# Kernel optimization log

Measured on AMD Instinct MI355X. Metric: run time of the kernel, lower is better.

Reference implementation:

```python
import jax, jax.numpy as jnp
import numpy as np

B, L, IN_DIM, D_MODEL, N_LAYERS = 4, 1024, 64, 512, 3
D_INNER, STATE, DT_RANK, K = 1024, 16, 32, 4  # expand=2, dt_rank=d_model//16, conv kernel 4


def setup_inputs() -> dict:
    key = jax.random.key(0)
    ks = jax.random.split(key, 8)
    s = 0.02
    def rn(k, shp):
        return jax.random.normal(k, shp, jnp.float32) * s
    inp = {"x": jax.random.normal(ks[0], (B, L, IN_DIM), jnp.float32)}
    inp["input_w"] = rn(ks[1], (D_MODEL, IN_DIM)); inp["input_b"] = jnp.zeros((D_MODEL,), jnp.float32)
    inp["in_proj_w"] = rn(ks[2], (N_LAYERS, 2 * D_INNER, D_MODEL)); inp["in_proj_b"] = jnp.zeros((N_LAYERS, 2 * D_INNER), jnp.float32)
    inp["conv_w"] = rn(ks[3], (N_LAYERS, D_INNER, 1, K)); inp["conv_b"] = jnp.zeros((N_LAYERS, D_INNER), jnp.float32)
    inp["x_proj_w"] = rn(ks[4], (N_LAYERS, DT_RANK + 2 * STATE, D_INNER))
    inp["dt_proj_w"] = rn(ks[5], (N_LAYERS, D_INNER, DT_RANK)); inp["dt_proj_b"] = jnp.full((N_LAYERS, D_INNER), -4.0, jnp.float32)
    inp["A_log"] = jnp.tile(jnp.log(jnp.arange(1, STATE + 1, dtype=jnp.float32))[None, None, :], (N_LAYERS, D_INNER, 1))
    inp["D"] = jnp.ones((N_LAYERS, D_INNER), jnp.float32)
    inp["out_proj_w"] = rn(ks[6], (N_LAYERS, D_MODEL, D_INNER)); inp["out_proj_b"] = jnp.zeros((N_LAYERS, D_MODEL), jnp.float32)
    inp["ln_w"] = jnp.ones((N_LAYERS, D_MODEL), jnp.float32); inp["ln_b"] = jnp.zeros((N_LAYERS, D_MODEL), jnp.float32)
    return inp


def _layernorm(x, w, b):
    mu = jnp.mean(x, -1, keepdims=True)
    v = jnp.var(x, -1, keepdims=True)
    return (x - mu) * jax.lax.rsqrt(v + 1e-5) * w + b


def _mamba(u, iw, ib, cw, cb, xw, dw, db, A_log, Dp, ow, ob):
    # u: [B, L, d_model]
    xz = u @ iw.T + ib                          # [B, L, 2*d_inner]
    xp, z = jnp.split(xz, 2, axis=-1)
    # causal depthwise conv over time
    xc = jax.lax.conv_general_dilated(xp.transpose(0, 2, 1), cw, (1,), [(K - 1, 0)],
                                      feature_group_count=D_INNER,
                                      dimension_numbers=("NCH", "OIH", "NCH")) + cb[None, :, None]
    xc = jax.nn.silu(xc).transpose(0, 2, 1)     # [B, L, d_inner]
    proj = xc @ xw.T                            # [B, L, dt_rank + 2*N]
    dtl = proj[..., :DT_RANK]
    Bm = proj[..., DT_RANK:DT_RANK + STATE]
    Cm = proj[..., DT_RANK + STATE:]
    dt = jax.nn.softplus(dtl @ dw.T + db)       # [B, L, d_inner]
    A = -jnp.exp(A_log)                         # [d_inner, N]

    def step(h, t):
        dt_t, B_t, C_t, x_t = t                 # [B,d], [B,N], [B,N], [B,d]
        h = h * jnp.exp(dt_t[..., None] * A) + (dt_t * x_t)[..., None] * B_t[:, None, :]
        return h, jnp.einsum("bdn,bn->bd", h, C_t)

    h0 = jnp.zeros((u.shape[0], D_INNER, STATE), u.dtype)
    _, ys = jax.lax.scan(step, h0, (dt.transpose(1, 0, 2), Bm.transpose(1, 0, 2),
                                    Cm.transpose(1, 0, 2), xc.transpose(1, 0, 2)))
    y = ys.transpose(1, 0, 2) + xc * Dp
    y = y * jax.nn.silu(z)
    return y @ ow.T + ob


def reference(x, input_w, input_b, in_proj_w, in_proj_b, conv_w, conv_b, x_proj_w,
              dt_proj_w, dt_proj_b, A_log, D, out_proj_w, out_proj_b, ln_w, ln_b):
    h = x @ input_w.T + input_b                 # [B, L, d_model]
    for i in range(N_LAYERS):
        res = h
        h = _mamba(h, in_proj_w[i], in_proj_b[i], conv_w[i], conv_b[i], x_proj_w[i],
                   dt_proj_w[i], dt_proj_b[i], A_log[i], D[i], out_proj_w[i], out_proj_b[i])
        h = _layernorm(h + res, ln_w[i], ln_b[i])
    return h[:, -1, :]
```

## Files before the change

### kernel.cpp

```cpp
#include <hip/hip_runtime.h>
#include <hip/hip_bf16.h>
#include <cstddef>
#include <cstdint>

#define NB 4
#define NL 1024
#define IN_DIM 64
#define D_MODEL 512
#define N_LAYERS 3
#define D_INNER 1024
#define NSTATE 16
#define DT_RANK 32
#define KCONV 4
#define NROWS (NB * NL)
#define CHUNK 16
#define NCHUNK (NL / CHUNK)
#define LOG2E 1.4426950408889634f

typedef __attribute__((ext_vector_type(8))) short short8;
typedef __attribute__((ext_vector_type(4))) float f32x4;
typedef __attribute__((ext_vector_type(4))) unsigned short us4;
typedef unsigned short ushort_t;

__device__ __forceinline__ ushort_t f2b1(float x) {
  uint32_t u = __builtin_bit_cast(uint32_t, x);
  u += 0x7fffu + ((u >> 16) & 1u);
  return (ushort_t)(u >> 16);
}
__device__ __forceinline__ float b2f(ushort_t u) {
  return __builtin_bit_cast(float, (uint32_t)u << 16);
}

__device__ __forceinline__ void gload_lds16(const ushort_t* src, short* dst) {
  __builtin_amdgcn_global_load_lds(
      (const __attribute__((address_space(1))) uint32_t*)src,
      (__attribute__((address_space(3))) uint32_t*)dst, 16, 0, 0);
}

#define E0 (NROWS * IN_DIM)
#define E1 (D_MODEL * IN_DIM)
#define E2 (N_LAYERS * 2 * D_INNER * D_MODEL)
#define E3 (N_LAYERS * 64 * D_INNER)
#define E4 (N_LAYERS * D_INNER * DT_RANK)
#define E5 (N_LAYERS * D_MODEL * D_INNER)
#define ETOT (E0 + E1 + E2 + E3 + E4 + E5)

__global__ __launch_bounds__(256) void cvt_all(
    const float* __restrict__ x, const float* __restrict__ inw,
    const float* __restrict__ ipw, const float* __restrict__ xpw,
    const float* __restrict__ dpw, const float* __restrict__ opw,
    ushort_t* __restrict__ xb, ushort_t* __restrict__ inwb,
    ushort_t* __restrict__ iwb, ushort_t* __restrict__ xwb,
    ushort_t* __restrict__ dwb, ushort_t* __restrict__ owb)
{
  int i = (blockIdx.x * 256 + threadIdx.x) * 4;
  if (i >= ETOT) return;
  const float* src; ushort_t* dst; int off;
  if      (i < E0)                  { src = x;   dst = xb;   off = i; }
  else if (i < E0+E1)               { src = inw; dst = inwb; off = i - E0; }
  else if (i < E0+E1+E2)            { src = ipw; dst = iwb;  off = i - (E0+E1); }
  else if (i < E0+E1+E2+E3)         { src = xpw; dst = xwb;  off = i - (E0+E1+E2); }
  else if (i < E0+E1+E2+E3+E4)      { src = dpw; dst = dwb;  off = i - (E0+E1+E2+E3); }
  else                              { src = opw; dst = owb;  off = i - (E0+E1+E2+E3+E4); }
  const float4 v = *(const float4*)(src + off);
  us4 o;
  o.x = f2b1(v.x); o.y = f2b1(v.y); o.z = f2b1(v.z); o.w = f2b1(v.w);
  *(us4*)(dst + off) = o;
}

template<int BM, int BN, int MF, int NF, int ACT, bool WF32, bool WB16>
__global__ __launch_bounds__(256) void gemm_mfma(
    const ushort_t* __restrict__ A, int lda,
    const ushort_t* __restrict__ W,
    const float* __restrict__ bias,
    float* __restrict__ Cf, ushort_t* __restrict__ Cb,
    int M, int N, int K)
{
  constexpr int CA = BM / 64;
  constexpr int CB = BN / 64;
  __shared__ __align__(16) short sa[BM * 32];
  __shared__ __align__(16) short sb[BN * 32];

  const int tid = threadIdx.x;
  const int l = tid & 63;
  const int wid = tid >> 6;
  const int wrow = (wid >> 1) * (BM / 2);
  const int wcol = (wid & 1) * (BN / 2);
  const int m0 = blockIdx.y * BM;
  const int n0 = blockIdx.x * BN;

  const int srow = l >> 2;
  const int scol = (l & 3) * 8;

  f32x4 acc[MF][NF] = {};

  for (int k0 = 0; k0 < K; k0 += 32) {
#pragma unroll
    for (int c = 0; c < CA; ++c) {
      short* dst = sa + (c * 4 + wid) * 512;
      const ushort_t* src =
          A + (size_t)(m0 + (c * 4 + wid) * 16 + srow) * lda + k0 + scol;
      gload_lds16(src, dst);
    }
#pragma unroll
    for (int c = 0; c < CB; ++c) {
      short* dst = sb + (c * 4 + wid) * 512;
      const ushort_t* src =
          W + (size_t)(n0 + (c * 4 + wid) * 16 + srow) * K + k0 + scol;
      gload_lds16(src, dst);
    }
    __syncthreads();

    short8 af[MF], bfr[NF];
#pragma unroll
    for (int mi = 0; mi < MF; ++mi)
      af[mi] = *(const short8*)(sa + (wrow + mi * 16 + (l & 15)) * 32 + (l >> 4) * 8);
#pragma unroll
    for (int nj = 0; nj < NF; ++nj)
      bfr[nj] = *(const short8*)(sb + (wcol + nj * 16 + (l & 15)) * 32 + (l >> 4) * 8);
#pragma unroll
    for (int mi = 0; mi < MF; ++mi)
#pragma unroll
      for (int nj = 0; nj < NF; ++nj)
        acc[mi][nj] = __builtin_amdgcn_mfma_f32_16x16x32_bf16(
            af[mi], bfr[nj], acc[mi][nj], 0, 0, 0);
    __syncthreads();
  }

#pragma unroll
  for (int nj = 0; nj < NF; ++nj) {
    const int col = n0 + wcol + nj * 16 + (l & 15);
    const float bv = bias ? bias[col] : 0.f;
#pragma unroll
    for (int mi = 0; mi < MF; ++mi) {
#pragma unroll
      for (int q = 0; q < 4; ++q) {
        const int row = m0 + wrow + mi * 16 + (l >> 4) * 4 + q;
        float v = acc[mi][nj][q] + bv;
        if (ACT == 1) v = (v > 20.f) ? v : log1pf(__expf(v));
        if (WF32) Cf[(size_t)row * N + col] = v;
        if (WB16) Cb[(size_t)row * N + col] = f2b1(v);
      }
    }
  }
}

__global__ __launch_bounds__(256) void conv_silu(
    const ushort_t* __restrict__ xzb,
    const float* __restrict__ cw,
    const float* __restrict__ cb,
    ushort_t* __restrict__ xcb)
{
  const int idx = blockIdx.x * 256 + threadIdx.x;
  const int d4 = (idx & (D_INNER / 4 - 1)) * 4;
  const int bt = idx >> 8;
  const int t = bt & (NL - 1);
  const int b = bt >> 10;

  float acc4[4];
  {
    const float4 cbv = *(const float4*)(cb + d4);
    acc4[0] = cbv.x; acc4[1] = cbv.y; acc4[2] = cbv.z; acc4[3] = cbv.w;
  }
  float wv[4][4];
#pragma unroll
  for (int i = 0; i < 4; ++i) {
    const float4 w = *(const float4*)(cw + (size_t)(d4 + i) * KCONV);
    wv[i][0] = w.x; wv[i][1] = w.y; wv[i][2] = w.z; wv[i][3] = w.w;
  }
#pragma unroll
  for (int j = 0; j < KCONV; ++j) {
    const int tt = t - (KCONV - 1) + j;
    if (tt >= 0) {
      const us4 xv = *(const us4*)(xzb + (size_t)(b * NL + tt) * (2 * D_INNER) + d4);
      acc4[0] = fmaf(b2f(xv.x), wv[0][j], acc4[0]);
      acc4[1] = fmaf(b2f(xv.y), wv[1][j], acc4[1]);
      acc4[2] = fmaf(b2f(xv.z), wv[2][j], acc4[2]);
      acc4[3] = fmaf(b2f(xv.w), wv[3][j], acc4[3]);
    }
  }
  us4 o;
#pragma unroll
  for (int i = 0; i < 4; ++i) {
    const float s = acc4[i] / (1.f + __expf(-acc4[i]));
    ((ushort_t*)&o)[i] = f2b1(s);
  }
  *(us4*)(xcb + (size_t)idx * 4) = o;
}

__global__ __launch_bounds__(256) void scan_phase1(
    const ushort_t* __restrict__ dtb,
    const float* __restrict__ proj,
    const ushort_t* __restrict__ xcb,
    const float* __restrict__ A_log,
    float* __restrict__ S_loc,
    float* __restrict__ sumdt)
{
  const int d = blockIdx.x * 256 + threadIdx.x;
  const int c = blockIdx.y;
  const int b = blockIdx.z;

  float A2[NSTATE];
#pragma unroll
  for (int n = 0; n < NSTATE; ++n)
    A2[n] = -__expf(A_log[d * NSTATE + n]) * LOG2E;

  float h[NSTATE];
#pragma unroll
  for (int n = 0; n < NSTATE; ++n) h[n] = 0.f;
  float sdt = 0.f;

  const int t0 = c * CHUNK;
#pragma unroll 4
  for (int tt = 0; tt < CHUNK; ++tt) {
    const size_t row = (size_t)(b * NL + t0 + tt);
    const float dtv = b2f(dtb[row * D_INNER + d]);
    const float xv = b2f(xcb[row * D_INNER + d]);
    const float* pr = proj + row * 64;
    float Bv[NSTATE];
    *(float4*)(Bv)      = *(const float4*)(pr + 32);
    *(float4*)(Bv + 4)  = *(const float4*)(pr + 36);
    *(float4*)(Bv + 8)  = *(const float4*)(pr + 40);
    *(float4*)(Bv + 12) = *(const float4*)(pr + 44);
    sdt += dtv;
    const float dx = dtv * xv;
#pragma unroll
    for (int n = 0; n < NSTATE; ++n)
      h[n] = fmaf(h[n], exp2f(dtv * A2[n]), dx * Bv[n]);
  }

  const size_t cbase = (size_t)(b * NCHUNK + c);
  sumdt[cbase * D_INNER + d] = sdt;
#pragma unroll
  for (int n = 0; n < NSTATE; ++n)
    S_loc[(cbase * NSTATE + n) * D_INNER + d] = h[n];
}

__global__ __launch_bounds__(256) void scan_carry(
    const float* __restrict__ S_loc,
    const float* __restrict__ sumdt,
    const float* __restrict__ A_log,
    float* __restrict__ H_in)
{
  const int idx = blockIdx.x * 256 + threadIdx.x;
  const int d = idx & (D_INNER - 1);
  const int n = (idx >> 10) & (NSTATE - 1);
  const int b = idx >> 14;

  const float A2n = -__expf(A_log[d * NSTATE + n]) * LOG2E;

  float H = 0.f;
  for (int c = 0; c < NCHUNK; ++c) {
    const size_t cbase = (size_t)(b * NCHUNK + c);
    H_in[(cbase * NSTATE + n) * D_INNER + d] = H;
    const float sdt = sumdt[cbase * D_INNER + d];
    H = fmaf(H, exp2f(A2n * sdt), S_loc[(cbase * NSTATE + n) * D_INNER + d]);
  }
}

__global__ __launch_bounds__(256) void scan_phase2(
    const ushort_t* __restrict__ dtb,
    const float* __restrict__ proj,
    const ushort_t* __restrict__ xcb,
    const ushort_t* __restrict__ xzb,
    const float* __restrict__ A_log,
    const float* __restrict__ Dp,
    const float* __restrict__ H_in,
    ushort_t* __restrict__ yb)
{
  const int d = blockIdx.x * 256 + threadIdx.x;
  const int c = blockIdx.y;
  const int b = blockIdx.z;

  float A2[NSTATE];
#pragma unroll
  for (int n = 0; n < NSTATE; ++n)
    A2[n] = -__expf(A_log[d * NSTATE + n]) * LOG2E;

  const size_t cbase = (size_t)(b * NCHUNK + c);
  float h[NSTATE];
#pragma unroll
  for (int n = 0; n < NSTATE; ++n)
    h[n] = H_in[(cbase * NSTATE + n) * D_INNER + d];

  const float Dv = Dp[d];
  const int t0 = c * CHUNK;

#pragma unroll 4
  for (int tt = 0; tt < CHUNK; ++tt) {
    const size_t row = (size_t)(b * NL + t0 + tt);
    const size_t rd = row * D_INNER + d;
    const float dtv = b2f(dtb[rd]);
    const float xv = b2f(xcb[rd]);
    const float* pr = proj + row * 64;
    float Bv[NSTATE], Cv[NSTATE];
    *(float4*)(Bv)      = *(const float4*)(pr + 32);
    *(float4*)(Bv + 4)  = *(const float4*)(pr + 36);
    *(float4*)(Bv + 8)  = *(const float4*)(pr + 40);
    *(float4*)(Bv + 12) = *(const float4*)(pr + 44);
    *(float4*)(Cv)      = *(const float4*)(pr + 48);
    *(float4*)(Cv + 4)  = *(const float4*)(pr + 52);
    *(float4*)(Cv + 8)  = *(const float4*)(pr + 56);
    *(float4*)(Cv + 12) = *(const float4*)(pr + 60);
    const float dx = dtv * xv;
    float accv = 0.f;
#pragma unroll
    for (int n = 0; n < NSTATE; ++n) {
      h[n] = fmaf(h[n], exp2f(dtv * A2[n]), dx * Bv[n]);
      accv = fmaf(h[n], Cv[n], accv);
    }
    const float zv = b2f(xzb[row * (2 * D_INNER) + D_INNER + d]);
    float yv = fmaf(xv, Dv, accv);
    yv *= zv / (1.f + __expf(-zv));
    yb[rd] = f2b1(yv);
  }
}

__global__ __launch_bounds__(256) void add_ln(
    const float* __restrict__ x,
    const float* __restrict__ res,
    const float* __restrict__ w,
    const float* __restrict__ bln,
    float* __restrict__ out,
    ushort_t* __restrict__ outb,
    float* __restrict__ out2)
{
  const int wave = threadIdx.x >> 6;
  const int lane = threadIdx.x & 63;
  const int row = blockIdx.x * 4 + wave;
  const float* xr = x + (size_t)row * D_MODEL;
  const float* rr = res + (size_t)row * D_MODEL;

  float v[8];
  float s = 0.f, s2 = 0.f;
#pragma unroll
  for (int i = 0; i < 8; ++i) {
    const float t = xr[lane + i * 64] + rr[lane + i * 64];
    v[i] = t; s += t; s2 = fmaf(t, t, s2);
  }
#pragma unroll
  for (int off = 32; off; off >>= 1) {
    s += __shfl_xor(s, off);
    s2 += __shfl_xor(s2, off);
  }
  const float mean = s * (1.f / D_MODEL);
  const float var = s2 * (1.f / D_MODEL) - mean * mean;
  const float rstd = rsqrtf(var + 1e-5f);
  const bool last_t = (row & (NL - 1)) == (NL - 1);
#pragma unroll
  for (int i = 0; i < 8; ++i) {
    const int c = lane + i * 64;
    const float o = (v[i] - mean) * rstd * w[c] + bln[c];
    out[(size_t)row * D_MODEL + c] = o;
    outb[(size_t)row * D_MODEL + c] = f2b1(o);
    if (out2 && last_t) out2[(size_t)(row >> 10) * D_MODEL + c] = o;
  }
}

extern "C" void kernel_launch(void* const* d_in, const int* in_sizes, int n_in,
                              void* d_out, int out_size, void* d_ws, size_t ws_size,
                              hipStream_t stream)
{
  const float* x         = (const float*)d_in[0];
  const float* input_w   = (const float*)d_in[1];
  const float* input_b   = (const float*)d_in[2];
  const float* in_proj_w = (const float*)d_in[3];
  const float* in_proj_b = (const float*)d_in[4];
  const float* conv_w    = (const float*)d_in[5];
  const float* conv_b    = (const float*)d_in[6];
  const float* x_proj_w  = (const float*)d_in[7];
  const float* dt_proj_w = (const float*)d_in[8];
  const float* dt_proj_b = (const float*)d_in[9];
  const float* A_log     = (const float*)d_in[10];
  const float* Dp        = (const float*)d_in[11];
  const float* out_proj_w= (const float*)d_in[12];
  const float* out_proj_b= (const float*)d_in[13];
  const float* ln_w      = (const float*)d_in[14];
  const float* ln_b      = (const float*)d_in[15];

  float* p = (float*)d_ws;
  float* h0   = p; p += (size_t)NROWS * D_MODEL;
  float* h1   = p; p += (size_t)NROWS * D_MODEL;
  float* tmp  = p; p += (size_t)NROWS * D_MODEL;
  float* proj = p; p += (size_t)NROWS * 64;
  float* Sloc = p; p += (size_t)NB * NCHUNK * NSTATE * D_INNER;
  float* Hin  = p; p += (size_t)NB * NCHUNK * NSTATE * D_INNER;
  float* sdt  = p; p += (size_t)NB * NCHUNK * D_INNER;
  ushort_t* q = (ushort_t*)p;
  ushort_t* xzb   = q; q += (size_t)NROWS * 2 * D_INNER;
  ushort_t* xcb   = q; q += (size_t)NROWS * D_INNER;
  ushort_t* dtbb  = q; q += (size_t)NROWS * D_INNER;
  ushort_t* projb = q; q += (size_t)NROWS * 64;
  ushort_t* yb    = q; q += (size_t)NROWS * D_INNER;
  ushort_t* hb    = q; q += (size_t)NROWS * D_MODEL;
  ushort_t* xb    = q; q += (size_t)E0;
  ushort_t* inwb  = q; q += (size_t)E1;
  ushort_t* iwb   = q; q += (size_t)E2;
  ushort_t* xwb   = q; q += (size_t)E3;
  ushort_t* dwb   = q; q += (size_t)E4;
  ushort_t* owb   = q; q += (size_t)E5;

  cvt_all<<<(ETOT / 4 + 255) / 256, 256, 0, stream>>>(
      x, input_w, in_proj_w, x_proj_w, dt_proj_w, out_proj_w,
      xb, inwb, iwb, xwb, dwb, owb);

  gemm_mfma<64, 64, 2, 2, 0, true, true>
      <<<dim3(D_MODEL / 64, NROWS / 64), 256, 0, stream>>>(
      xb, IN_DIM, inwb, input_b, h0, hb, NROWS, D_MODEL, IN_DIM);

  float* hc = h0;
  float* hn = h1;

  for (int l = 0; l < N_LAYERS; ++l) {
    const ushort_t* iw = iwb + (size_t)l * 2 * D_INNER * D_MODEL;
    const float* ib = in_proj_b + (size_t)l * 2 * D_INNER;
    const float* cw = conv_w    + (size_t)l * D_INNER * KCONV;
    const float* cb = conv_b    + (size_t)l * D_INNER;
    const ushort_t* xw = xwb + (size_t)l * 64 * D_INNER;
    const ushort_t* dw = dwb + (size_t)l * D_INNER * DT_RANK;
    const float* db = dt_proj_b + (size_t)l * D_INNER;
    const float* Al = A_log     + (size_t)l * D_INNER * NSTATE;
    const float* Dl = Dp        + (size_t)l * D_INNER;
    const ushort_t* ow = owb + (size_t)l * D_MODEL * D_INNER;
    const float* ob = out_proj_b+ (size_t)l * D_MODEL;
    const float* lw = ln_w      + (size_t)l * D_MODEL;
    const float* lb = ln_b      + (size_t)l * D_MODEL;

    gemm_mfma<128, 128, 4, 4, 0, false, true>
        <<<dim3(2 * D_INNER / 128, NROWS / 128), 256, 0, stream>>>(
        hb, D_MODEL, iw, ib, nullptr, xzb, NROWS, 2 * D_INNER, D_MODEL);

    conv_silu<<<NROWS * D_INNER / 4 / 256, 256, 0, stream>>>(xzb, cw, cb, xcb);

    gemm_mfma<64, 64, 2, 2, 0, true, true>
        <<<dim3(1, NROWS / 64), 256, 0, stream>>>(
        xcb, D_INNER, xw, nullptr, proj, projb, NROWS, 64, D_INNER);

    gemm_mfma<128, 128, 4, 4, 1, false, true>
        <<<dim3(D_INNER / 128, NROWS / 128), 256, 0, stream>>>(
        projb, 64, dw, db, nullptr, dtbb, NROWS, D_INNER, DT_RANK);

    scan_phase1<<<dim3(D_INNER / 256, NCHUNK, NB), 256, 0, stream>>>(
        dtbb, proj, xcb, Al, Sloc, sdt);
    scan_carry<<<(NB * NSTATE * D_INNER) / 256, 256, 0, stream>>>(
        Sloc, sdt, Al, Hin);
    scan_phase2<<<dim3(D_INNER / 256, NCHUNK, NB), 256, 0, stream>>>(
        dtbb, proj, xcb, xzb, Al, Dl, Hin, yb);

    gemm_mfma<128, 128, 4, 4, 0, true, false>
        <<<dim3(D_MODEL / 128, NROWS / 128), 256, 0, stream>>>(
        yb, D_INNER, ow, ob, tmp, nullptr, NROWS, D_MODEL, D_INNER);

    add_ln<<<NROWS / 4, 256, 0, stream>>>(
        tmp, hc, lw, lb, hn, hb,
        (l == N_LAYERS - 1) ? (float*)d_out : nullptr);

    float* t2 = hc; hc = hn; hn = t2;
  }
}
```

Baseline: 599.4 us.

## Add BK template to MFMA GEMM with XOR-swizzled LDS, stage scan B/C in shared memory

The GEMM gains a K-tile template parameter, so most calls now load 64-wide K slices per barrier pair, halving the synchronisation count. An XOR swizzle on the LDS layout is meant to avoid bank conflicts. The out_proj GEMM switches to 64x128 tiles to launch more blocks. Both scan phases load each chunk's B/C projection rows into shared memory once, instead of every thread reading them from global memory each step, at the cost of an extra barrier and some LDS.

Result: slower. 776.8 us (+29.6%).

```diff
diff --git a/kernel.cpp b/kernel.cpp
--- a/kernel.cpp
+++ b/kernel.cpp
@@ -68,7 +68,7 @@
   *(us4*)(dst + off) = o;
 }
 
-template<int BM, int BN, int MF, int NF, int ACT, bool WF32, bool WB16>
+template<int BM, int BN, int BK, int MF, int NF, int ACT, bool WF32, bool WB16>
 __global__ __launch_bounds__(256) void gemm_mfma(
     const ushort_t* __restrict__ A, int lda,
     const ushort_t* __restrict__ W,
@@ -76,10 +76,12 @@
     float* __restrict__ Cf, ushort_t* __restrict__ Cb,
     int M, int N, int K)
 {
-  constexpr int CA = BM / 64;
-  constexpr int CB = BN / 64;
-  __shared__ __align__(16) short sa[BM * 32];
-  __shared__ __align__(16) short sb[BN * 32];
+  constexpr int CPR = BK / 8;
+  constexpr int CA = BM * CPR / 256;
+  constexpr int CB = BN * CPR / 256;
+  constexpr int KK = BK / 32;
+  __shared__ __align__(16) short sa[BM * BK];
+  __shared__ __align__(16) short sb[BN * BK];
 
   const int tid = threadIdx.x;
   const int l = tid & 63;
@@ -89,41 +91,49 @@
   const int m0 = blockIdx.y * BM;
   const int n0 = blockIdx.x * BN;
 
-  const int srow = l >> 2;
-  const int scol = (l & 3) * 8;
-
   f32x4 acc[MF][NF] = {};
 
-  for (int k0 = 0; k0 < K; k0 += 32) {
+  for (int k0 = 0; k0 < K; k0 += BK) {
 #pragma unroll
     for (int c = 0; c < CA; ++c) {
+      const int slot = (c * 4 + wid) * 64 + l;
+      const int r = slot / CPR, c16 = slot % CPR;
+      const int s16 = c16 ^ (r & (CPR - 1));
       short* dst = sa + (c * 4 + wid) * 512;
-      const ushort_t* src =
-          A + (size_t)(m0 + (c * 4 + wid) * 16 + srow) * lda + k0 + scol;
-      gload_lds16(src, dst);
+      gload_lds16(A + (size_t)(m0 + r) * lda + k0 + s16 * 8, dst);
     }
 #pragma unroll
     for (int c = 0; c < CB; ++c) {
+      const int slot = (c * 4 + wid) * 64 + l;
+      const int r = slot / CPR, c16 = slot % CPR;
+      const int s16 = c16 ^ (r & (CPR - 1));
       short* dst = sb + (c * 4 + wid) * 512;
-      const ushort_t* src =
-          W + (size_t)(n0 + (c * 4 + wid) * 16 + srow) * K + k0 + scol;
-      gload_lds16(src, dst);
+      gload_lds16(W + (size_t)(n0 + r) * K + k0 + s16 * 8, dst);
     }
     __syncthreads();
 
-    short8 af[MF], bfr[NF];
-#pragma unroll
-    for (int mi = 0; mi < MF; ++mi)
-      af[mi] = *(const short8*)(sa + (wrow + mi * 16 + (l & 15)) * 32 + (l >> 4) * 8);
-#pragma unroll
-    for (int nj = 0; nj < NF; ++nj)
-      bfr[nj] = *(const short8*)(sb + (wcol + nj * 16 + (l & 15)) * 32 + (l >> 4) * 8);
-#pragma unroll
-    for (int mi = 0; mi < MF; ++mi)
-#pragma unroll
-      for (int nj = 0; nj < NF; ++nj)
-        acc[mi][nj] = __builtin_amdgcn_mfma_f32_16x16x32_bf16(
-            af[mi], bfr[nj], acc[mi][nj], 0, 0, 0);
+#pragma unroll
+    for (int kk = 0; kk < KK; ++kk) {
+      short8 af[MF], bfr[NF];
+#pragma unroll
+      for (int mi = 0; mi < MF; ++mi) {
+        const int r = wrow + mi * 16 + (l & 15);
+        const int cc = (kk * 4 + (l >> 4)) ^ (r & (CPR - 1));
+        af[mi] = *(const short8*)(sa + r * BK + cc * 8);
+      }
+#pragma unroll
+      for (int nj = 0; nj < NF; ++nj) {
+        const int r = wcol + nj * 16 + (l & 15);
+        const int cc = (kk * 4 + (l >> 4)) ^ (r & (CPR - 1));
+        bfr[nj] = *(const short8*)(sb + r * BK + cc * 8);
+      }
+#pragma unroll
+      for (int mi = 0; mi < MF; ++mi)
+#pragma unroll
+        for (int nj = 0; nj < NF; ++nj)
+          acc[mi][nj] = __builtin_amdgcn_mfma_f32_16x16x32_bf16(
+              af[mi], bfr[nj], acc[mi][nj], 0, 0, 0);
+    }
     __syncthreads();
   }
 
@@ -196,9 +206,19 @@
     float* __restrict__ S_loc,
     float* __restrict__ sumdt)
 {
+  __shared__ float prs[CHUNK][64];
   const int d = blockIdx.x * 256 + threadIdx.x;
   const int c = blockIdx.y;
   const int b = blockIdx.z;
+  const int t0 = c * CHUNK;
+
+#pragma unroll
+  for (int i = 0; i < 4; ++i) {
+    const int idx = i * 256 + threadIdx.x;
+    prs[idx >> 6][idx & 63] =
+        proj[((size_t)(b * NL + t0) + (idx >> 6)) * 64 + (idx & 63)];
+  }
+  __syncthreads();
 
   float A2[NSTATE];
 #pragma unroll
@@ -210,18 +230,16 @@
   for (int n = 0; n < NSTATE; ++n) h[n] = 0.f;
   float sdt = 0.f;
 
-  const int t0 = c * CHUNK;
 #pragma unroll 4
   for (int tt = 0; tt < CHUNK; ++tt) {
     const size_t row = (size_t)(b * NL + t0 + tt);
     const float dtv = b2f(dtb[row * D_INNER + d]);
     const float xv = b2f(xcb[row * D_INNER + d]);
-    const float* pr = proj + row * 64;
     float Bv[NSTATE];
-    *(float4*)(Bv)      = *(const float4*)(pr + 32);
-    *(float4*)(Bv + 4)  = *(const float4*)(pr + 36);
-    *(float4*)(Bv + 8)  = *(const float4*)(pr + 40);
-    *(float4*)(Bv + 12) = *(const float4*)(pr + 44);
+    *(float4*)(Bv)      = *(const float4*)(&prs[tt][32]);
+    *(float4*)(Bv + 4)  = *(const float4*)(&prs[tt][36]);
+    *(float4*)(Bv + 8)  = *(const float4*)(&prs[tt][40]);
+    *(float4*)(Bv + 12) = *(const float4*)(&prs[tt][44]);
     sdt += dtv;
     const float dx = dtv * xv;
 #pragma unroll
@@ -268,9 +286,19 @@
     const float* __restrict__ H_in,
     ushort_t* __restrict__ yb)
 {
+  __shared__ float prs[CHUNK][64];
   const int d = blockIdx.x * 256 + threadIdx.x;
   const int c = blockIdx.y;
   const int b = blockIdx.z;
+  const int t0 = c * CHUNK;
+
+#pragma unroll
+  for (int i = 0; i < 4; ++i) {
+    const int idx = i * 256 + threadIdx.x;
+    prs[idx >> 6][idx & 63] =
+        proj[((size_t)(b * NL + t0) + (idx >> 6)) * 64 + (idx & 63)];
+  }
+  __syncthreads();
 
   float A2[NSTATE];
 #pragma unroll
@@ -284,7 +312,6 @@
     h[n] = H_in[(cbase * NSTATE + n) * D_INNER + d];
 
   const float Dv = Dp[d];
-  const int t0 = c * CHUNK;
 
 #pragma unroll 4
   for (int tt = 0; tt < CHUNK; ++tt) {
@@ -292,16 +319,15 @@
     const size_t rd = row * D_INNER + d;
     const float dtv = b2f(dtb[rd]);
     const float xv = b2f(xcb[rd]);
-    const float* pr = proj + row * 64;
     float Bv[NSTATE], Cv[NSTATE];
-    *(float4*)(Bv)      = *(const float4*)(pr + 32);
-    *(float4*)(Bv + 4)  = *(const float4*)(pr + 36);
-    *(float4*)(Bv + 8)  = *(const float4*)(pr + 40);
-    *(float4*)(Bv + 12) = *(const float4*)(pr + 44);
-    *(float4*)(Cv)      = *(const float4*)(pr + 48);
-    *(float4*)(Cv + 4)  = *(const float4*)(pr + 52);
-    *(float4*)(Cv + 8)  = *(const float4*)(pr + 56);
-    *(float4*)(Cv + 12) = *(const float4*)(pr + 60);
+    *(float4*)(Bv)      = *(const float4*)(&prs[tt][32]);
+    *(float4*)(Bv + 4)  = *(const float4*)(&prs[tt][36]);
+    *(float4*)(Bv + 8)  = *(const float4*)(&prs[tt][40]);
+    *(float4*)(Bv + 12) = *(const float4*)(&prs[tt][44]);
+    *(float4*)(Cv)      = *(const float4*)(&prs[tt][48]);
+    *(float4*)(Cv + 4)  = *(const float4*)(&prs[tt][52]);
+    *(float4*)(Cv + 8)  = *(const float4*)(&prs[tt][56]);
+    *(float4*)(Cv + 12) = *(const float4*)(&prs[tt][60]);
     const float dx = dtv * xv;
     float accv = 0.f;
 #pragma unroll
@@ -404,7 +430,7 @@
       x, input_w, in_proj_w, x_proj_w, dt_proj_w, out_proj_w,
       xb, inwb, iwb, xwb, dwb, owb);
 
-  gemm_mfma<64, 64, 2, 2, 0, true, true>
+  gemm_mfma<64, 64, 64, 2, 2, 0, true, true>
       <<<dim3(D_MODEL / 64, NROWS / 64), 256, 0, stream>>>(
       xb, IN_DIM, inwb, input_b, h0, hb, NROWS, D_MODEL, IN_DIM);
 
@@ -426,17 +452,17 @@
     const float* lw = ln_w      + (size_t)l * D_MODEL;
     const float* lb = ln_b      + (size_t)l * D_MODEL;
 
-    gemm_mfma<128, 128, 4, 4, 0, false, true>
+    gemm_mfma<128, 128, 64, 4, 4, 0, false, true>
         <<<dim3(2 * D_INNER / 128, NROWS / 128), 256, 0, stream>>>(
         hb, D_MODEL, iw, ib, nullptr, xzb, NROWS, 2 * D_INNER, D_MODEL);
 
     conv_silu<<<NROWS * D_INNER / 4 / 256, 256, 0, stream>>>(xzb, cw, cb, xcb);
 
-    gemm_mfma<64, 64, 2, 2, 0, true, true>
+    gemm_mfma<64, 64, 64, 2, 2, 0, true, true>
         <<<dim3(1, NROWS / 64), 256, 0, stream>>>(
         xcb, D_INNER, xw, nullptr, proj, projb, NROWS, 64, D_INNER);
 
-    gemm_mfma<128, 128, 4, 4, 1, false, true>
+    gemm_mfma<128, 128, 32, 4, 4, 1, false, true>
         <<<dim3(D_INNER / 128, NROWS / 128), 256, 0, stream>>>(
         projb, 64, dw, db, nullptr, dtbb, NROWS, D_INNER, DT_RANK);
 
@@ -447,8 +473,8 @@
     scan_phase2<<<dim3(D_INNER / 256, NCHUNK, NB), 256, 0, stream>>>(
         dtbb, proj, xcb, xzb, Al, Dl, Hin, yb);
 
-    gemm_mfma<128, 128, 4, 4, 0, true, false>
-        <<<dim3(D_MODEL / 128, NROWS / 128), 256, 0, stream>>>(
+    gemm_mfma<64, 128, 64, 2, 4, 0, true, false>
+        <<<dim3(D_MODEL / 128, NROWS / 64), 256, 0, stream>>>(
         yb, D_INNER, ow, ob, tmp, nullptr, NROWS, D_MODEL, D_INNER);
 
     add_ln<<<NROWS / 4, 256, 0, stream>>>(
```
